# Kernel optimization log

Hardware: AMD Instinct MI355X
Metric: run time of the kernel (lower is better)

Reference implementation:

```python
import jax, jax.numpy as jnp
import numpy as np

B, I, J, D_IN, D_INNER = 128, 1024, 1024, 256, 256


def setup_inputs() -> dict:
    key = jax.random.key(0)
    ks = jax.random.split(key, 6)
    std = 0.02
    return {
        "q": jax.random.normal(ks[0], (B, I, D_IN), dtype=jnp.float32),
        "k": jax.random.normal(ks[1], (B, J, D_IN), dtype=jnp.float32),
        "v": jax.random.normal(ks[2], (B, J, D_IN), dtype=jnp.float32),
        # torch nn.Linear weights: shape [out_features, in_features]
        "Wq": jax.random.normal(ks[3], (D_INNER, D_IN), dtype=jnp.float32) * std,
        "Wk": jax.random.normal(ks[4], (D_INNER, D_IN), dtype=jnp.float32) * std,
        "Wv": jax.random.normal(ks[5], (D_INNER, D_IN), dtype=jnp.float32) * std,
    }


def reference(q, k, v, Wq, Wk, Wv):
    # Linear projections (bias=False): x @ W.T
    qh = jnp.einsum('bid,ed->bie', q, Wq)  # [B, I, D_INNER]
    kh = jnp.einsum('bjd,ed->bje', k, Wk)  # [B, J, D_INNER]
    vh = jnp.einsum('bjd,ed->bje', v, Wv)  # [B, J, D_INNER] (embed_frame=True)
    scale = jnp.asarray(D_INNER, qh.dtype) ** -0.5  # heads == 1
    dots = jnp.einsum('bid,bjd->bij', qh, kh) * scale  # [B, I, J]
    attn = jax.nn.softmax(dots, axis=-1)
    out = jnp.einsum('bij,bjd->bid', attn, vh)  # [B, I, D_INNER]
    return out
```

## Files before the change

kernel.cpp:

```cpp
#include <hip/hip_runtime.h>
#include <stdint.h>


typedef __attribute__((ext_vector_type(4))) float f32x4;
typedef __attribute__((ext_vector_type(8))) short bf16x8;
typedef __attribute__((ext_vector_type(4))) uint32_t u32x4;
typedef __attribute__((ext_vector_type(4))) short s16x4;

#define MFMA(a, b, c) __builtin_amdgcn_mfma_f32_16x16x32_bf16(a, b, c, 0, 0, 0)

typedef const __attribute__((address_space(1))) uint32_t* gas1_t;
typedef __attribute__((address_space(3))) uint32_t* las3_t;

__device__ __forceinline__ void async16(const void* g, void* l) {
  __builtin_amdgcn_global_load_lds((gas1_t)g, (las3_t)l, 16, 0, 0);
}

__device__ __forceinline__ short f2bf_rne(float f) {
  uint32_t u = __builtin_bit_cast(uint32_t, f);
  u += 0x7FFFu + ((u >> 16) & 1u);
  return (short)(u >> 16);
}

__device__ __forceinline__ uint32_t pack2(float lo, float hi) {
  uint32_t a = __builtin_bit_cast(uint32_t, lo);
  uint32_t b = __builtin_bit_cast(uint32_t, hi);
  return (a >> 16) | (b & 0xFFFF0000u);
}

__device__ __forceinline__ void wait_barrier() {
  __builtin_amdgcn_sched_barrier(0);
  asm volatile("s_waitcnt vmcnt(0)" ::: "memory");
  __builtin_amdgcn_s_barrier();
  __builtin_amdgcn_sched_barrier(0);
}

__global__ __launch_bounds__(256)
void wconv_kernel(const float* __restrict__ wq, const float* __restrict__ wk,
                  const float* __restrict__ wv, short* __restrict__ wbf) {
  const int mat = blockIdx.y;
  const float* w = (mat == 0) ? wq : (mat == 1) ? wk : wv;
  const int i = (blockIdx.x * 256 + threadIdx.x) * 4;
  f32x4 v = *(const f32x4*)(w + i);
  s16x4 o = {f2bf_rne(v.x), f2bf_rne(v.y), f2bf_rne(v.z), f2bf_rne(v.w)};
  *(s16x4*)(wbf + (size_t)mat * 65536 + i) = o;
}

__global__ __launch_bounds__(512)
void proj_kernel(const float* __restrict__ xq, const float* __restrict__ xk,
                 const float* __restrict__ xv, const short* __restrict__ wbf,
                 short* __restrict__ qh, short* __restrict__ kh,
                 short* __restrict__ vt) {
  __shared__ __align__(16) char smem[65536];
  short* ldst = (short*)smem;

  const int mat = blockIdx.y;
  const float* x = (mat == 0) ? xq : (mat == 1) ? xk : xv;
  const short* w = wbf + (size_t)mat * 65536;

  const int tile_m = blockIdx.x * 128;
  const int t = threadIdx.x;
  const int lane = t & 63, wid = t >> 6;
  const int wm = (wid & 1) * 64, wn = (wid >> 1) * 64;
  const int lr = lane & 15, lq = lane >> 4;

  f32x4 acc[4][4];
#pragma unroll
  for (int i = 0; i < 4; ++i)
#pragma unroll
    for (int j = 0; j < 4; ++j) acc[i][j] = (f32x4)0.0f;

  auto STAGE = [&](int kk, int h) {
    char* base = smem + h * 32768;
    const int k0 = kk * 32;
#pragma unroll
    for (int c = 0; c < 2; ++c) {
      int s = c * 512 + t;
      int rx = ((s >> 7) << 4) | (s & 15);
      int cx = (s >> 4) & 7;
      async16(x + (size_t)(tile_m + rx) * 256 + k0 + cx * 4, base + s * 16);
      int rw = ((s >> 6) << 4) | (s & 15);
      int cw = (s >> 4) & 3;
      async16(w + (size_t)rw * 256 + k0 + cw * 8, base + 16384 + s * 16);
    }
  };

  STAGE(0, 0);
  wait_barrier();
  int cur = 0;
  for (int kk = 0; kk < 8; ++kk) {
    if (kk < 7) STAGE(kk + 1, cur ^ 1);
    const f32x4* x4 = (const f32x4*)(smem + cur * 32768);
    const f32x4* w4 = (const f32x4*)(smem + cur * 32768 + 16384);
    bf16x8 af[4], bf[4];
#pragma unroll
    for (int mi = 0; mi < 4; ++mi) {
      int row = wm + mi * 16 + lr;
      int sl = ((row >> 4) << 7) + (lq << 5) + (row & 15);
      f32x4 lo = x4[sl], hi = x4[sl + 16];
      u32x4 pk = {pack2(lo.x, lo.y), pack2(lo.z, lo.w), pack2(hi.x, hi.y),
                  pack2(hi.z, hi.w)};
      af[mi] = __builtin_bit_cast(bf16x8, pk);
    }
#pragma unroll
    for (int ni = 0; ni < 4; ++ni) {
      int col = wn + ni * 16 + lr;
      bf[ni] = __builtin_bit_cast(
          bf16x8, w4[((col >> 4) << 6) + (lq << 4) + (col & 15)]);
    }
    __builtin_amdgcn_s_setprio(1);
#pragma unroll
    for (int mi = 0; mi < 4; ++mi)
#pragma unroll
      for (int ni = 0; ni < 4; ++ni)
        acc[mi][ni] = MFMA(af[mi], bf[ni], acc[mi][ni]);
    __builtin_amdgcn_s_setprio(0);
    wait_barrier();
    cur ^= 1;
  }

  const float scale = (mat == 0) ? 0.0625f : 1.0f;
  const int bb = tile_m >> 10, j0 = tile_m & 1023;
#pragma unroll
  for (int p = 0; p < 2; ++p) {
    if (((wid >> 1) >> 1) == p) {
#pragma unroll
      for (int mi = 0; mi < 4; ++mi)
#pragma unroll
        for (int ni = 0; ni < 4; ++ni)
#pragma unroll
          for (int r = 0; r < 4; ++r) {
            int m = wm + mi * 16 + lq * 4 + r;
            int n = ((wid >> 1) & 1) * 64 + ni * 16 + lr;
            short bv = f2bf_rne(acc[mi][ni][r] * scale);
            if (mat < 2) ldst[m * 136 + n] = bv;
            else         ldst[n * 136 + m] = bv;
          }
    }
    __syncthreads();
#pragma unroll
    for (int q = 0; q < 4; ++q) {
      int idx = q * 512 + t;
      int row = idx >> 4;
      int col8 = (idx & 15) * 8;
      bf16x8 vdat = *(const bf16x8*)(ldst + row * 136 + col8);
      short* dst;
      if (mat < 2) {
        short* o = (mat == 0) ? qh : kh;
        dst = o + (size_t)(tile_m + row) * 256 + p * 128 + col8;
      } else {
        dst = vt + ((size_t)(bb * 256 + p * 128 + row)) * 1024 + j0 + col8;
      }
      *(bf16x8*)dst = vdat;
    }
    __syncthreads();
  }
}

__global__ __launch_bounds__(512)
void attn_kernel(const short* __restrict__ qh, const short* __restrict__ kh,
                 const short* __restrict__ vt, float* __restrict__ out) {
  __shared__ __align__(16) char smem[32768 + 34816];
  short* ldsS = (short*)smem;
  short* ldsP = (short*)(smem + 32768);

  const int b = blockIdx.x;
  const int i0 = blockIdx.y * 128;
  const int t = threadIdx.x;
  const int lane = t & 63, wid = t >> 6;
  const int rg = wid >> 1, cg = wid & 1;
  const int lr = lane & 15, lq = lane >> 4;
  const size_t bq = (size_t)b * 262144;

  f32x4 oacc[2][8];
#pragma unroll
  for (int i = 0; i < 2; ++i)
#pragma unroll
    for (int j = 0; j < 8; ++j) oacc[i][j] = (f32x4)0.0f;
  float lsum[8];
#pragma unroll
  for (int i = 0; i < 8; ++i) lsum[i] = 0.0f;

  auto STAGE_QK = [&](int jt, int kk, int h) {
    short* base = ldsS + h * 8192;
    const int j0 = jt * 128, k0 = kk * 32;
    int s = t;
    int r = ((s >> 6) << 4) | (s & 15);
    int c8 = (s >> 4) & 3;
    async16(qh + bq + (size_t)(i0 + r) * 256 + k0 + c8 * 8, base + s * 8);
    async16(kh + bq + (size_t)(j0 + r) * 256 + k0 + c8 * 8, base + 4096 + s * 8);
  };
  auto STAGE_V = [&](int jt, int kc, int h) {
    short* base = ldsS + h * 8192;
    const int j0 = jt * 128;
#pragma unroll
    for (int c = 0; c < 2; ++c) {
      int s = c * 512 + t;
      int d = ((s >> 6) << 4) | (s & 15);
      int c8 = (s >> 4) & 3;
      async16(vt + bq + (size_t)d * 1024 + j0 + kc * 32 + c8 * 8, base + s * 8);
    }
  };

  STAGE_QK(0, 0, 0);
  wait_barrier();
  int cur = 0;

  for (int jt = 0; jt < 8; ++jt) {
    f32x4 sacc[2][4];
#pragma unroll
    for (int i = 0; i < 2; ++i)
#pragma unroll
      for (int j = 0; j < 4; ++j) sacc[i][j] = (f32x4)0.0f;

    for (int kk = 0; kk < 8; ++kk) {
      if (kk < 7) STAGE_QK(jt, kk + 1, cur ^ 1);
      else        STAGE_V(jt, 0, cur ^ 1);
      const f32x4* q4 = (const f32x4*)(ldsS + cur * 8192);
      const f32x4* k4 = q4 + 512;
      bf16x8 aq[2], bk[4];
#pragma unroll
      for (int mi = 0; mi < 2; ++mi) {
        int row = rg * 32 + mi * 16 + lr;
        aq[mi] = __builtin_bit_cast(
            bf16x8, q4[((row >> 4) << 6) + (lq << 4) + (row & 15)]);
      }
#pragma unroll
      for (int ni = 0; ni < 4; ++ni) {
        int col = cg * 64 + ni * 16 + lr;
        bk[ni] = __builtin_bit_cast(
            bf16x8, k4[((col >> 4) << 6) + (lq << 4) + (col & 15)]);
      }
      __builtin_amdgcn_s_setprio(1);
#pragma unroll
      for (int mi = 0; mi < 2; ++mi)
#pragma unroll
        for (int ni = 0; ni < 4; ++ni)
          sacc[mi][ni] = MFMA(aq[mi], bk[ni], sacc[mi][ni]);
      __builtin_amdgcn_s_setprio(0);
      wait_barrier();
      cur ^= 1;
    }

    float prt[8];
#pragma unroll
    for (int i = 0; i < 8; ++i) prt[i] = 0.0f;
#pragma unroll
    for (int mi = 0; mi < 2; ++mi)
#pragma unroll
      for (int ni = 0; ni < 4; ++ni)
#pragma unroll
        for (int r = 0; r < 4; ++r) {
          float e = __expf(sacc[mi][ni][r]);
          prt[mi * 4 + r] += e;
          int m = rg * 32 + mi * 16 + lq * 4 + r;
          int jc = cg * 64 + ni * 16 + lr;
          ldsP[m * 136 + jc] = f2bf_rne(e);
        }
#pragma unroll
    for (int v = 0; v < 8; ++v) {
      float p = prt[v];
      p += __shfl_xor(p, 1, 64);
      p += __shfl_xor(p, 2, 64);
      p += __shfl_xor(p, 4, 64);
      p += __shfl_xor(p, 8, 64);
      lsum[v] += p;
    }
    __syncthreads();

    for (int kc = 0; kc < 4; ++kc) {
      if (kc < 3)      STAGE_V(jt, kc + 1, cur ^ 1);
      else if (jt < 7) STAGE_QK(jt + 1, 0, cur ^ 1);
      const f32x4* v4 = (const f32x4*)(ldsS + cur * 8192);
      const f32x4* p4 = (const f32x4*)ldsP;
      bf16x8 pf[2], vf[8];
#pragma unroll
      for (int mi = 0; mi < 2; ++mi) {
        int m = rg * 32 + mi * 16 + lr;
        pf[mi] = __builtin_bit_cast(bf16x8, p4[m * 17 + kc * 4 + lq]);
      }
#pragma unroll
      for (int ni = 0; ni < 8; ++ni) {
        int d = cg * 128 + ni * 16 + lr;
        vf[ni] = __builtin_bit_cast(
            bf16x8, v4[((d >> 4) << 6) + (lq << 4) + (d & 15)]);
      }
      __builtin_amdgcn_s_setprio(1);
#pragma unroll
      for (int mi = 0; mi < 2; ++mi)
#pragma unroll
        for (int ni = 0; ni < 8; ++ni)
          oacc[mi][ni] = MFMA(pf[mi], vf[ni], oacc[mi][ni]);
      __builtin_amdgcn_s_setprio(0);
      wait_barrier();
      cur ^= 1;
    }
  }

  float* lscr = (float*)ldsP;
  if (lr == 0) {
#pragma unroll
    for (int mi = 0; mi < 2; ++mi)
#pragma unroll
      for (int r = 0; r < 4; ++r)
        lscr[wid * 32 + mi * 16 + lq * 4 + r] = lsum[mi * 4 + r];
  }
  __syncthreads();
  float inv[8];
#pragma unroll
  for (int mi = 0; mi < 2; ++mi)
#pragma unroll
    for (int r = 0; r < 4; ++r) {
      float tot = lsum[mi * 4 + r] + lscr[(wid ^ 1) * 32 + mi * 16 + lq * 4 + r];
      inv[mi * 4 + r] = 1.0f / tot;
    }
#pragma unroll
  for (int mi = 0; mi < 2; ++mi)
#pragma unroll
    for (int ni = 0; ni < 8; ++ni)
#pragma unroll
      for (int r = 0; r < 4; ++r) {
        int i = i0 + rg * 32 + mi * 16 + lq * 4 + r;
        int d = cg * 128 + ni * 16 + lr;
        out[bq + (size_t)i * 256 + d] = oacc[mi][ni][r] * inv[mi * 4 + r];
      }
}

extern "C" void kernel_launch(void* const* d_in, const int* in_sizes, int n_in,
                              void* d_out, int out_size, void* d_ws,
                              size_t ws_size, hipStream_t stream) {
  (void)in_sizes; (void)n_in; (void)out_size; (void)ws_size;
  const float* q  = (const float*)d_in[0];
  const float* k  = (const float*)d_in[1];
  const float* v  = (const float*)d_in[2];
  const float* wq = (const float*)d_in[3];
  const float* wk = (const float*)d_in[4];
  const float* wv = (const float*)d_in[5];
  float* out = (float*)d_out;

  short* qh = (short*)d_ws;
  short* kh = qh + (size_t)33554432;
  short* vt = kh + (size_t)33554432;
  short* wbf = (short*)d_out;

  wconv_kernel<<<dim3(64, 3), dim3(256), 0, stream>>>(wq, wk, wv, wbf);
  proj_kernel<<<dim3(1024, 3), dim3(512), 0, stream>>>(
      q, k, v, wbf, qh, kh, vt);
  attn_kernel<<<dim3(128, 8), dim3(512), 0, stream>>>(qh, kh, vt, out);
}
```

Measured before the change: 828.8 us.

## Split staging into half-size units with a 4-slot ring and partial vmcnt waits

Both the projection and attention kernels now issue async global-to-LDS loads in finer units (Q/K or X/W halves, V halves) cycling through a 4-slot LDS ring. Barriers use s_waitcnt vmcnt(N) with N>0, so later loads stay in flight while earlier units are consumed, instead of draining everything before each barrier. The aim is deeper prefetch and less exposed load latency. The cost is more barriers per iteration and more complex slot indexing, with ordering risks around the P-tile writes, which now use only an lgkmcnt wait.

```diff
diff --git a/kernel.cpp b/kernel.cpp
--- a/kernel.cpp
+++ b/kernel.cpp
@@ -28,9 +28,15 @@
   return (a >> 16) | (b & 0xFFFF0000u);
 }
 
-__device__ __forceinline__ void wait_barrier() {
+template <int N>
+__device__ __forceinline__ void unit_wait() {
   __builtin_amdgcn_sched_barrier(0);
-  asm volatile("s_waitcnt vmcnt(0)" ::: "memory");
+  if constexpr (N == 0)
+    asm volatile("s_waitcnt vmcnt(0)" ::: "memory");
+  else if constexpr (N == 1)
+    asm volatile("s_waitcnt vmcnt(1)" ::: "memory");
+  else
+    asm volatile("s_waitcnt vmcnt(2)" ::: "memory");
   __builtin_amdgcn_s_barrier();
   __builtin_amdgcn_sched_barrier(0);
 }
@@ -70,28 +76,39 @@
 #pragma unroll
     for (int j = 0; j < 4; ++j) acc[i][j] = (f32x4)0.0f;
 
-  auto STAGE = [&](int kk, int h) {
-    char* base = smem + h * 32768;
-    const int k0 = kk * 32;
-#pragma unroll
-    for (int c = 0; c < 2; ++c) {
-      int s = c * 512 + t;
-      int rx = ((s >> 7) << 4) | (s & 15);
-      int cx = (s >> 4) & 7;
-      async16(x + (size_t)(tile_m + rx) * 256 + k0 + cx * 4, base + s * 16);
-      int rw = ((s >> 6) << 4) | (s & 15);
-      int cw = (s >> 4) & 3;
-      async16(w + (size_t)rw * 256 + k0 + cw * 8, base + 16384 + s * 16);
+  auto ISSUE = [&](int u) {
+    if (u >= 16) return;
+    char* base = smem + (u & 3) * 16384;
+    const int k0 = (u >> 1) * 32;
+    if ((u & 1) == 0) {
+#pragma unroll
+      for (int c = 0; c < 2; ++c) {
+        int s = c * 512 + t;
+        int rx = ((s >> 7) << 4) | (s & 15);
+        int cx = (s >> 4) & 7;
+        async16(x + (size_t)(tile_m + rx) * 256 + k0 + cx * 4, base + s * 16);
+      }
+    } else {
+#pragma unroll
+      for (int c = 0; c < 2; ++c) {
+        int s = c * 512 + t;
+        int rw = ((s >> 6) << 4) | (s & 15);
+        int cw = (s >> 4) & 3;
+        async16(w + (size_t)rw * 256 + k0 + cw * 8, base + s * 16);
+      }
     }
   };
 
-  STAGE(0, 0);
-  wait_barrier();
-  int cur = 0;
+  ISSUE(0);
+  ISSUE(1);
   for (int kk = 0; kk < 8; ++kk) {
-    if (kk < 7) STAGE(kk + 1, cur ^ 1);
-    const f32x4* x4 = (const f32x4*)(smem + cur * 32768);
-    const f32x4* w4 = (const f32x4*)(smem + cur * 32768 + 16384);
+    const int u = kk * 2 + 1;
+    unit_wait<2>();
+    ISSUE(u + 1);
+    if (kk == 7) unit_wait<0>(); else unit_wait<2>();
+    ISSUE(u + 2);
+    const f32x4* x4 = (const f32x4*)(smem + ((u - 1) & 3) * 16384);
+    const f32x4* w4 = (const f32x4*)(smem + (u & 3) * 16384);
     bf16x8 af[4], bf[4];
 #pragma unroll
     for (int mi = 0; mi < 4; ++mi) {
@@ -115,9 +132,8 @@
       for (int ni = 0; ni < 4; ++ni)
         acc[mi][ni] = MFMA(af[mi], bf[ni], acc[mi][ni]);
     __builtin_amdgcn_s_setprio(0);
-    wait_barrier();
-    cur ^= 1;
   }
+  __syncthreads();
 
   const float scale = (mat == 0) ? 0.0625f : 1.0f;
   const int bb = tile_m >> 10, j0 = tile_m & 1023;
@@ -181,30 +197,32 @@
 #pragma unroll
   for (int i = 0; i < 8; ++i) lsum[i] = 0.0f;
 
-  auto STAGE_QK = [&](int jt, int kk, int h) {
-    short* base = ldsS + h * 8192;
-    const int j0 = jt * 128, k0 = kk * 32;
-    int s = t;
-    int r = ((s >> 6) << 4) | (s & 15);
-    int c8 = (s >> 4) & 3;
-    async16(qh + bq + (size_t)(i0 + r) * 256 + k0 + c8 * 8, base + s * 8);
-    async16(kh + bq + (size_t)(j0 + r) * 256 + k0 + c8 * 8, base + 4096 + s * 8);
-  };
-  auto STAGE_V = [&](int jt, int kc, int h) {
-    short* base = ldsS + h * 8192;
+  auto ISSUE = [&](int u) {
+    if (u >= 192) return;
+    short* base = ldsS + (u & 3) * 4096;
+    const int jt = u / 24, r = u % 24;
     const int j0 = jt * 128;
-#pragma unroll
-    for (int c = 0; c < 2; ++c) {
-      int s = c * 512 + t;
-      int d = ((s >> 6) << 4) | (s & 15);
+    const int s = t;
+    if (r < 16) {
+      const int k0 = (r >> 1) * 32;
+      int rr = ((s >> 6) << 4) | (s & 15);
+      int c8 = (s >> 4) & 3;
+      if ((r & 1) == 0)
+        async16(qh + bq + (size_t)(i0 + rr) * 256 + k0 + c8 * 8, base + s * 8);
+      else
+        async16(kh + bq + (size_t)(j0 + rr) * 256 + k0 + c8 * 8, base + s * 8);
+    } else {
+      const int v = r - 16;
+      const int kc = v >> 1, half = v & 1;
+      int d = (half << 7) | ((s >> 6) << 4) | (s & 15);
       int c8 = (s >> 4) & 3;
       async16(vt + bq + (size_t)d * 1024 + j0 + kc * 32 + c8 * 8, base + s * 8);
     }
   };
 
-  STAGE_QK(0, 0, 0);
-  wait_barrier();
-  int cur = 0;
+  ISSUE(0);
+  ISSUE(1);
+  int u = 0;
 
   for (int jt = 0; jt < 8; ++jt) {
     f32x4 sacc[2][4];
@@ -214,10 +232,13 @@
       for (int j = 0; j < 4; ++j) sacc[i][j] = (f32x4)0.0f;
 
     for (int kk = 0; kk < 8; ++kk) {
-      if (kk < 7) STAGE_QK(jt, kk + 1, cur ^ 1);
-      else        STAGE_V(jt, 0, cur ^ 1);
-      const f32x4* q4 = (const f32x4*)(ldsS + cur * 8192);
-      const f32x4* k4 = q4 + 512;
+      unit_wait<1>();
+      ISSUE(u + 2);
+      ++u;
+      unit_wait<1>();
+      ISSUE(u + 2);
+      const f32x4* q4 = (const f32x4*)(ldsS + ((u - 1) & 3) * 4096);
+      const f32x4* k4 = (const f32x4*)(ldsS + (u & 3) * 4096);
       bf16x8 aq[2], bk[4];
 #pragma unroll
       for (int mi = 0; mi < 2; ++mi) {
@@ -238,8 +259,7 @@
         for (int ni = 0; ni < 4; ++ni)
           sacc[mi][ni] = MFMA(aq[mi], bk[ni], sacc[mi][ni]);
       __builtin_amdgcn_s_setprio(0);
-      wait_barrier();
-      cur ^= 1;
+      ++u;
     }
 
     float prt[8];
@@ -266,12 +286,16 @@
       p += __shfl_xor(p, 8, 64);
       lsum[v] += p;
     }
-    __syncthreads();
+    asm volatile("s_waitcnt lgkmcnt(0)" ::: "memory");
 
     for (int kc = 0; kc < 4; ++kc) {
-      if (kc < 3)      STAGE_V(jt, kc + 1, cur ^ 1);
-      else if (jt < 7) STAGE_QK(jt + 1, 0, cur ^ 1);
-      const f32x4* v4 = (const f32x4*)(ldsS + cur * 8192);
+      unit_wait<1>();
+      ISSUE(u + 2);
+      ++u;
+      if (jt == 7 && kc == 3) unit_wait<0>(); else unit_wait<1>();
+      ISSUE(u + 2);
+      const f32x4* v4 =
+          (const f32x4*)(ldsS + ((cg ? u : (u - 1)) & 3) * 4096);
       const f32x4* p4 = (const f32x4*)ldsP;
       bf16x8 pf[2], vf[8];
 #pragma unroll
@@ -281,9 +305,7 @@
       }
 #pragma unroll
       for (int ni = 0; ni < 8; ++ni) {
-        int d = cg * 128 + ni * 16 + lr;
-        vf[ni] = __builtin_bit_cast(
-            bf16x8, v4[((d >> 4) << 6) + (lq << 4) + (d & 15)]);
+        vf[ni] = __builtin_bit_cast(bf16x8, v4[ni * 64 + (lq << 4) + lr]);
       }
       __builtin_amdgcn_s_setprio(1);
 #pragma unroll
@@ -292,10 +314,10 @@
         for (int ni = 0; ni < 8; ++ni)
           oacc[mi][ni] = MFMA(pf[mi], vf[ni], oacc[mi][ni]);
       __builtin_amdgcn_s_setprio(0);
-      wait_barrier();
-      cur ^= 1;
+      ++u;
     }
   }
+  __syncthreads();
 
   float* lscr = (float*)ldsP;
   if (lr == 0) {
```

Result: faster. 738.6 us (-10.9%).

## Replace LDS-staged async double-buffering with direct global-to-register operand loads

Applied to the files above, without the earlier changes.

Removes the global_load_lds double-buffered staging of Q, K, V and the projection inputs. MFMA operands are now read straight from global memory into registers, and LDS is kept only for the softmax P tile and the output transpose. This drops the per-step barriers and shrinks LDS use, which could allow more resident blocks. The cost is that data shared across waves is no longer reused through LDS, so global and L2 traffic rises, and the loads are less coalesced (strided rows of 16 bytes per lane).

```diff
diff --git a/kernel.cpp b/kernel.cpp
--- a/kernel.cpp
+++ b/kernel.cpp
@@ -9,13 +9,6 @@
 
 #define MFMA(a, b, c) __builtin_amdgcn_mfma_f32_16x16x32_bf16(a, b, c, 0, 0, 0)
 
-typedef const __attribute__((address_space(1))) uint32_t* gas1_t;
-typedef __attribute__((address_space(3))) uint32_t* las3_t;
-
-__device__ __forceinline__ void async16(const void* g, void* l) {
-  __builtin_amdgcn_global_load_lds((gas1_t)g, (las3_t)l, 16, 0, 0);
-}
-
 __device__ __forceinline__ short f2bf_rne(float f) {
   uint32_t u = __builtin_bit_cast(uint32_t, f);
   u += 0x7FFFu + ((u >> 16) & 1u);
@@ -26,13 +19,6 @@
   uint32_t a = __builtin_bit_cast(uint32_t, lo);
   uint32_t b = __builtin_bit_cast(uint32_t, hi);
   return (a >> 16) | (b & 0xFFFF0000u);
-}
-
-__device__ __forceinline__ void wait_barrier() {
-  __builtin_amdgcn_sched_barrier(0);
-  asm volatile("s_waitcnt vmcnt(0)" ::: "memory");
-  __builtin_amdgcn_s_barrier();
-  __builtin_amdgcn_sched_barrier(0);
 }
 
 __global__ __launch_bounds__(256)
@@ -51,8 +37,7 @@
                  const float* __restrict__ xv, const short* __restrict__ wbf,
                  short* __restrict__ qh, short* __restrict__ kh,
                  short* __restrict__ vt) {
-  __shared__ __align__(16) char smem[65536];
-  short* ldst = (short*)smem;
+  __shared__ __align__(16) short ldst[128 * 136];
 
   const int mat = blockIdx.y;
   const float* x = (mat == 0) ? xq : (mat == 1) ? xk : xv;
@@ -70,44 +55,24 @@
 #pragma unroll
     for (int j = 0; j < 4; ++j) acc[i][j] = (f32x4)0.0f;
 
-  auto STAGE = [&](int kk, int h) {
-    char* base = smem + h * 32768;
-    const int k0 = kk * 32;
-#pragma unroll
-    for (int c = 0; c < 2; ++c) {
-      int s = c * 512 + t;
-      int rx = ((s >> 7) << 4) | (s & 15);
-      int cx = (s >> 4) & 7;
-      async16(x + (size_t)(tile_m + rx) * 256 + k0 + cx * 4, base + s * 16);
-      int rw = ((s >> 6) << 4) | (s & 15);
-      int cw = (s >> 4) & 3;
-      async16(w + (size_t)rw * 256 + k0 + cw * 8, base + 16384 + s * 16);
-    }
-  };
-
-  STAGE(0, 0);
-  wait_barrier();
-  int cur = 0;
+  const float* xb = x + (size_t)(tile_m + wm + lr) * 256 + lq * 8;
+  const short* wb = w + (size_t)(wn + lr) * 256 + lq * 8;
+
+#pragma unroll
   for (int kk = 0; kk < 8; ++kk) {
-    if (kk < 7) STAGE(kk + 1, cur ^ 1);
-    const f32x4* x4 = (const f32x4*)(smem + cur * 32768);
-    const f32x4* w4 = (const f32x4*)(smem + cur * 32768 + 16384);
     bf16x8 af[4], bf[4];
 #pragma unroll
     for (int mi = 0; mi < 4; ++mi) {
-      int row = wm + mi * 16 + lr;
-      int sl = ((row >> 4) << 7) + (lq << 5) + (row & 15);
-      f32x4 lo = x4[sl], hi = x4[sl + 16];
+      const float* p = xb + (size_t)mi * 16 * 256 + kk * 32;
+      f32x4 lo = *(const f32x4*)p;
+      f32x4 hi = *(const f32x4*)(p + 4);
       u32x4 pk = {pack2(lo.x, lo.y), pack2(lo.z, lo.w), pack2(hi.x, hi.y),
                   pack2(hi.z, hi.w)};
       af[mi] = __builtin_bit_cast(bf16x8, pk);
     }
 #pragma unroll
-    for (int ni = 0; ni < 4; ++ni) {
-      int col = wn + ni * 16 + lr;
-      bf[ni] = __builtin_bit_cast(
-          bf16x8, w4[((col >> 4) << 6) + (lq << 4) + (col & 15)]);
-    }
+    for (int ni = 0; ni < 4; ++ni)
+      bf[ni] = *(const bf16x8*)(wb + (size_t)ni * 16 * 256 + kk * 32);
     __builtin_amdgcn_s_setprio(1);
 #pragma unroll
     for (int mi = 0; mi < 4; ++mi)
@@ -115,9 +80,8 @@
       for (int ni = 0; ni < 4; ++ni)
         acc[mi][ni] = MFMA(af[mi], bf[ni], acc[mi][ni]);
     __builtin_amdgcn_s_setprio(0);
-    wait_barrier();
-    cur ^= 1;
-  }
+  }
+  __syncthreads();
 
   const float scale = (mat == 0) ? 0.0625f : 1.0f;
   const int bb = tile_m >> 10, j0 = tile_m & 1023;
@@ -160,9 +124,7 @@
 __global__ __launch_bounds__(512)
 void attn_kernel(const short* __restrict__ qh, const short* __restrict__ kh,
                  const short* __restrict__ vt, float* __restrict__ out) {
-  __shared__ __align__(16) char smem[32768 + 34816];
-  short* ldsS = (short*)smem;
-  short* ldsP = (short*)(smem + 32768);
+  __shared__ __align__(16) short ldsP[128 * 136];
 
   const int b = blockIdx.x;
   const int i0 = blockIdx.y * 128;
@@ -181,56 +143,31 @@
 #pragma unroll
   for (int i = 0; i < 8; ++i) lsum[i] = 0.0f;
 
-  auto STAGE_QK = [&](int jt, int kk, int h) {
-    short* base = ldsS + h * 8192;
-    const int j0 = jt * 128, k0 = kk * 32;
-    int s = t;
-    int r = ((s >> 6) << 4) | (s & 15);
-    int c8 = (s >> 4) & 3;
-    async16(qh + bq + (size_t)(i0 + r) * 256 + k0 + c8 * 8, base + s * 8);
-    async16(kh + bq + (size_t)(j0 + r) * 256 + k0 + c8 * 8, base + 4096 + s * 8);
-  };
-  auto STAGE_V = [&](int jt, int kc, int h) {
-    short* base = ldsS + h * 8192;
+  const short* qb = qh + bq + (size_t)(i0 + rg * 32 + lr) * 256 + lq * 8;
+  const short* kb = kh + bq + (size_t)(cg * 64 + lr) * 256 + lq * 8;
+  const short* vb = vt + bq + (size_t)(cg * 128 + lr) * 1024 + lq * 8;
+  const f32x4* p4 = (const f32x4*)ldsP;
+
+  for (int jt = 0; jt < 8; ++jt) {
     const int j0 = jt * 128;
-#pragma unroll
-    for (int c = 0; c < 2; ++c) {
-      int s = c * 512 + t;
-      int d = ((s >> 6) << 4) | (s & 15);
-      int c8 = (s >> 4) & 3;
-      async16(vt + bq + (size_t)d * 1024 + j0 + kc * 32 + c8 * 8, base + s * 8);
-    }
-  };
-
-  STAGE_QK(0, 0, 0);
-  wait_barrier();
-  int cur = 0;
-
-  for (int jt = 0; jt < 8; ++jt) {
+    __syncthreads();
+
     f32x4 sacc[2][4];
 #pragma unroll
     for (int i = 0; i < 2; ++i)
 #pragma unroll
       for (int j = 0; j < 4; ++j) sacc[i][j] = (f32x4)0.0f;
 
+    const short* kbj = kb + (size_t)j0 * 256;
+#pragma unroll
     for (int kk = 0; kk < 8; ++kk) {
-      if (kk < 7) STAGE_QK(jt, kk + 1, cur ^ 1);
-      else        STAGE_V(jt, 0, cur ^ 1);
-      const f32x4* q4 = (const f32x4*)(ldsS + cur * 8192);
-      const f32x4* k4 = q4 + 512;
       bf16x8 aq[2], bk[4];
 #pragma unroll
-      for (int mi = 0; mi < 2; ++mi) {
-        int row = rg * 32 + mi * 16 + lr;
-        aq[mi] = __builtin_bit_cast(
-            bf16x8, q4[((row >> 4) << 6) + (lq << 4) + (row & 15)]);
-      }
-#pragma unroll
-      for (int ni = 0; ni < 4; ++ni) {
-        int col = cg * 64 + ni * 16 + lr;
-        bk[ni] = __builtin_bit_cast(
-            bf16x8, k4[((col >> 4) << 6) + (lq << 4) + (col & 15)]);
-      }
+      for (int mi = 0; mi < 2; ++mi)
+        aq[mi] = *(const bf16x8*)(qb + (size_t)mi * 16 * 256 + kk * 32);
+#pragma unroll
+      for (int ni = 0; ni < 4; ++ni)
+        bk[ni] = *(const bf16x8*)(kbj + (size_t)ni * 16 * 256 + kk * 32);
       __builtin_amdgcn_s_setprio(1);
 #pragma unroll
       for (int mi = 0; mi < 2; ++mi)
@@ -238,8 +175,6 @@
         for (int ni = 0; ni < 4; ++ni)
           sacc[mi][ni] = MFMA(aq[mi], bk[ni], sacc[mi][ni]);
       __builtin_amdgcn_s_setprio(0);
-      wait_barrier();
-      cur ^= 1;
     }
 
     float prt[8];
@@ -268,11 +203,8 @@
     }
     __syncthreads();
 
+#pragma unroll
     for (int kc = 0; kc < 4; ++kc) {
-      if (kc < 3)      STAGE_V(jt, kc + 1, cur ^ 1);
-      else if (jt < 7) STAGE_QK(jt + 1, 0, cur ^ 1);
-      const f32x4* v4 = (const f32x4*)(ldsS + cur * 8192);
-      const f32x4* p4 = (const f32x4*)ldsP;
       bf16x8 pf[2], vf[8];
 #pragma unroll
       for (int mi = 0; mi < 2; ++mi) {
@@ -280,11 +212,8 @@
         pf[mi] = __builtin_bit_cast(bf16x8, p4[m * 17 + kc * 4 + lq]);
       }
 #pragma unroll
-      for (int ni = 0; ni < 8; ++ni) {
-        int d = cg * 128 + ni * 16 + lr;
-        vf[ni] = __builtin_bit_cast(
-            bf16x8, v4[((d >> 4) << 6) + (lq << 4) + (d & 15)]);
-      }
+      for (int ni = 0; ni < 8; ++ni)
+        vf[ni] = *(const bf16x8*)(vb + (size_t)ni * 16 * 1024 + j0 + kc * 32);
       __builtin_amdgcn_s_setprio(1);
 #pragma unroll
       for (int mi = 0; mi < 2; ++mi)
@@ -292,10 +221,9 @@
         for (int ni = 0; ni < 8; ++ni)
           oacc[mi][ni] = MFMA(pf[mi], vf[ni], oacc[mi][ni]);
       __builtin_amdgcn_s_setprio(0);
-      wait_barrier();
-      cur ^= 1;
-    }
-  }
+    }
+  }
+  __syncthreads();
 
   float* lscr = (float*)ldsP;
   if (lr == 0) {
```

After: 1.133 ms. 1.37x slower.
